# Optimization experiments

Measured on AMD Instinct MI355X. Metric: run time of the kernel, lower is better.

## Reference

```python
import jax, jax.numpy as jnp
import numpy as np

B, N, N_IN, MSG_HID, MSG_OUT, N_HID, N_OUT, K = 32, 128, 16, 64, 64, 64, 16, 4
E = N * (N - 1)  # 16256 directed edges, fully connected w/o self-loops


def setup_inputs() -> dict:
    key = jax.random.key(0)
    ks = jax.random.split(key, 8)
    # one-hot relation matrices (NRI convention)
    rows, cols = np.where(np.ones((N, N)) - np.eye(N))
    eye = np.eye(N, dtype=np.float32)
    rel_rec = jnp.asarray(eye[rows])   # [E, N]
    rel_send = jnp.asarray(eye[cols])  # [E, N]
    s = 0.1  # weight init scale
    return {
        "inputs": jax.random.normal(ks[0], (B, N_IN, N), jnp.float32),
        "rel_rec": rel_rec,
        "rel_send": rel_send,
        "rel_types": jax.nn.softmax(jax.random.normal(ks[1], (B, E, K), jnp.float32), axis=-1),
        "W1": jax.random.normal(ks[2], (K, 2 * N_IN, MSG_HID), jnp.float32) * s,
        "b1": jnp.zeros((K, MSG_HID), jnp.float32),
        "W2": jax.random.normal(ks[3], (K, MSG_HID, MSG_OUT), jnp.float32) * s,
        "b2": jnp.zeros((K, MSG_OUT), jnp.float32),
        "Wo1": jax.random.normal(ks[4], (MSG_OUT + N_IN, N_HID), jnp.float32) * s,
        "bo1": jnp.zeros((N_HID,), jnp.float32),
        "Wo2": jax.random.normal(ks[5], (N_HID, N_HID), jnp.float32) * s,
        "bo2": jnp.zeros((N_HID,), jnp.float32),
        "Wo3": jax.random.normal(ks[6], (N_HID, N_OUT), jnp.float32) * s,
        "bo3": jnp.zeros((N_OUT,), jnp.float32),
    }


def reference(inputs, rel_rec, rel_send, rel_types, W1, b1, W2, b2, Wo1, bo1, Wo2, bo2, Wo3, bo3):
    x = jnp.transpose(inputs, (0, 2, 1))                     # [B, N, n_in]
    senders = jnp.einsum('en,bnf->bef', rel_send, x)          # [B, E, n_in]
    receivers = jnp.einsum('en,bnf->bef', rel_rec, x)         # [B, E, n_in]
    pre_msg = jnp.concatenate([senders, receivers], axis=-1)  # [B, E, 2*n_in]
    all_msgs = jnp.zeros((pre_msg.shape[0], pre_msg.shape[1], W2.shape[-1]), pre_msg.dtype)
    for k in range(W1.shape[0]):  # small fixed loop over edge types
        m = jax.nn.relu(pre_msg @ W1[k] + b1[k])
        m = jax.nn.relu(m @ W2[k] + b2[k])
        all_msgs = all_msgs + m * rel_types[:, :, k:k + 1]
    # edge2node aggregation (no normalization in forward path, matches source)
    agg_msgs = jnp.einsum('bem,en->bnm', all_msgs, rel_rec)   # [B, N, msg_out]
    aug_msgs = jnp.concatenate([x, agg_msgs], axis=-1)        # [B, N, n_in+msg_out]
    h = jax.nn.relu(aug_msgs @ Wo1 + bo1)  # dropout disabled (eval mode)
    h = jax.nn.relu(h @ Wo2 + bo2)
    pred = h @ Wo3 + bo3                                      # [B, N, n_out]
    return jnp.transpose(pred, (0, 2, 1))                     # [B, n_out, N]
```

## Files before the change

### kernel.cpp

```cpp
#include <hip/hip_runtime.h>
#include <stdint.h>

#define B_  32
#define N_  128
#define NIN 16
#define K_  4
#define E_  (N_*(N_-1))

typedef float    f4 __attribute__((ext_vector_type(4)));
typedef _Float16 h8 __attribute__((ext_vector_type(8)));
typedef _Float16 h4 __attribute__((ext_vector_type(4)));

__global__ __launch_bounds__(256) void prep(
    const float* __restrict__ inp, const float* __restrict__ W1,
    const float* __restrict__ b1,  const float* __restrict__ W2,
    const float* __restrict__ Wo1, const float* __restrict__ Wo2,
    const float* __restrict__ Wo3,
    _Float16* __restrict__ Sh, _Float16* __restrict__ Rh,
    _Float16* __restrict__ w2h, _Float16* __restrict__ wn)
{
    const int bid = blockIdx.x;
    const int tid = threadIdx.x;
    if (bid < 1024) {
        int gid = bid*256 + tid;
        int c0 = (gid & 15)*4;
        int n  = (gid >> 4) & 127;
        int b  = (gid >> 11) & 31;
        int k  = gid >> 16;
        f4 s = {0.f,0.f,0.f,0.f};
        f4 r = *(const f4*)(b1 + k*64 + c0);
        const float* xp  = inp + (b*NIN)*N_ + n;
        const f4* w1s = (const f4*)(W1 + (k*32)*64 + c0);
        const f4* w1r = (const f4*)(W1 + (k*32 + 16)*64 + c0);
        #pragma unroll
        for (int f = 0; f < 16; ++f) {
            float xv = xp[f*N_];
            s += xv * w1s[f*16];
            r += xv * w1r[f*16];
        }
        int base = ((k*B_ + b)*N_ + n)*64 + c0;
        h4 sh, rh;
        #pragma unroll
        for (int u = 0; u < 4; ++u) { sh[u] = (_Float16)s[u]; rh[u] = (_Float16)r[u]; }
        *(h4*)(Sh + base) = sh;
        *(h4*)(Rh + base) = rh;
    } else if (bid < 1088) {
        int t = (bid - 1024)*256 + tid;
        int i    = t & 7;
        int lane = (t >> 3) & 63;
        int nt   = (t >> 9) & 3;
        int ks   = (t >> 11) & 1;
        int k    = t >> 12;
        int c = ks*32 + (lane >> 4)*8 + i;
        int o = nt*16 + (lane & 15);
        w2h[t] = (_Float16)W2[(k*64 + c)*64 + o];
    } else {
        int t = (bid - 1088)*256 + tid;
        int j    = t & 7;
        int lane = (t >> 3) & 63;
        int f    = t >> 9;
        int col = lane & 15, q = lane >> 4, row = q*8 + j;
        float v;
        if (f < 12) {
            int ks = f >> 2, nt = f & 3, i = ks*32 + row;
            v = (i < 80) ? Wo1[i*64 + nt*16 + col] : 0.f;
        } else if (f < 20) {
            int g = f - 12, ks = g >> 2, nt = g & 3, i = ks*32 + row;
            v = Wo2[i*64 + nt*16 + col];
        } else {
            int ks = f - 20, i = ks*32 + row;
            v = Wo3[i*16 + col];
        }
        wn[t] = (_Float16)v;
    }
}

__global__ __launch_bounds__(512) void edge_mfma(
    const _Float16* __restrict__ Sh, const _Float16* __restrict__ Rh,
    const _Float16* __restrict__ w2h, const float* __restrict__ rt,
    const float* __restrict__ b2, float* __restrict__ aggK)
{
    __shared__ _Float16 Ssw[N_*64];

    const int tid  = threadIdx.x;
    const int wave = tid >> 6;
    const int lane = tid & 63;
    const int col  = lane & 15;
    const int q    = lane >> 4;
    const int bid  = blockIdx.x;
    const int rt4  = bid & 3;
    const int b    = (bid >> 2) & 31;
    const int k    = bid >> 7;
    const int kb   = k*B_ + b;

    const _Float16* Sg = Sh + (size_t)kb*(N_*64);
    #pragma unroll
    for (int rnd = 0; rnd < 2; ++rnd) {
        int p  = rnd*512 + tid;
        int s  = p >> 3;
        int c8 = (p & 7) ^ (s & 7);
        h8 v = *(const h8*)(Sg + (s*8 + c8)*8);
        *(h8*)(Ssw + p*8) = v;
    }

    const h8* w2v = (const h8*)w2h;
    h8 w2f[2][4];
    #pragma unroll
    for (int ks = 0; ks < 2; ++ks)
        #pragma unroll
        for (int nt = 0; nt < 4; ++nt)
            w2f[ks][nt] = w2v[((k*2 + ks)*4 + nt)*64 + lane];

    f4 b2i[4];
    #pragma unroll
    for (int nt = 0; nt < 4; ++nt) {
        float v = b2[k*64 + nt*16 + col];
        b2i[nt][0] = v; b2i[nt][1] = v; b2i[nt][2] = v; b2i[nt][3] = v;
    }

    __syncthreads();

    const h8* Rv = (const h8*)Rh;
    const h8 zero8 = {0,0,0,0,0,0,0,0};

    #pragma unroll 1
    for (int rg = 0; rg < 4; ++rg) {
        const int r = rt4*32 + wave*4 + rg;
        h8 rf0 = Rv[(kb*N_ + r)*8 + q];
        h8 rf1 = Rv[(kb*N_ + r)*8 + 4 + q];
        const float* rtb = rt + ((size_t)(b*E_ + r*127))*4 + k;

        float aggacc[4] = {0.f, 0.f, 0.f, 0.f};
        #pragma unroll
        for (int mt = 0; mt < 8; ++mt) {
            float rtv[4];
            #pragma unroll
            for (int i = 0; i < 4; ++i) {
                int sdx = mt*16 + q*4 + i;
                float v = 0.f;
                if (sdx != r) v = rtb[(sdx - (sdx > r ? 1 : 0))*4];
                rtv[i] = v;
            }
            int s  = mt*16 + col;
            int x0 = (s*8 + (q       ^ (s & 7)))*8;
            int x1 = (s*8 + ((4 + q) ^ (s & 7)))*8;
            h8 a0 = *(const h8*)(Ssw + x0);
            h8 a1 = *(const h8*)(Ssw + x1);
            a0 = __builtin_elementwise_max(a0 + rf0, zero8);
            a1 = __builtin_elementwise_max(a1 + rf1, zero8);

            #pragma unroll
            for (int nt = 0; nt < 4; ++nt) {
                f4 acc = __builtin_amdgcn_mfma_f32_16x16x32_f16(a0, w2f[0][nt], b2i[nt], 0, 0, 0);
                acc     = __builtin_amdgcn_mfma_f32_16x16x32_f16(a1, w2f[1][nt], acc,    0, 0, 0);
                #pragma unroll
                for (int i = 0; i < 4; ++i)
                    aggacc[nt] += rtv[i] * fmaxf(acc[i], 0.f);
            }
        }
        #pragma unroll
        for (int nt = 0; nt < 4; ++nt) {
            float v = aggacc[nt];
            v += __shfl_xor(v, 16, 64);
            v += __shfl_xor(v, 32, 64);
            if (lane < 16) aggK[((size_t)kb*N_ + r)*64 + nt*16 + lane] = v;
        }
    }
}

__global__ __launch_bounds__(256) void node_mfma(
    const float* __restrict__ aggK, const float* __restrict__ inp,
    const _Float16* __restrict__ wn,
    const float* __restrict__ bo1, const float* __restrict__ bo2,
    const float* __restrict__ bo3, float* __restrict__ out)
{
    __shared__ _Float16 augH[64*128];
    __shared__ _Float16 h12[64*64];

    const int tid = threadIdx.x;
    const int b   = blockIdx.x >> 1;
    const int r0  = (blockIdx.x & 1)*64;

    {
        const int nl = tid >> 2, c4 = tid & 3;
        const int r  = r0 + nl;
        float xv[4];
        #pragma unroll
        for (int u = 0; u < 4; ++u)
            xv[u] = inp[(b*NIN + c4*4 + u)*N_ + r];
        f4 av[4];
        #pragma unroll
        for (int w = 0; w < 4; ++w) {
            int c = w*16 + c4*4;
            f4 a = {0.f,0.f,0.f,0.f};
            #pragma unroll
            for (int k = 0; k < 4; ++k)
                a += *(const f4*)(aggK + (((size_t)k*B_ + b)*N_ + r)*64 + c);
            av[w] = a;
        }
        #pragma unroll
        for (int u = 0; u < 4; ++u) {
            int i = c4*4 + u;
            augH[nl*128 + (((i>>3) ^ (nl&15))<<3) + (i&7)] = (_Float16)xv[u];
        }
        #pragma unroll
        for (int w = 0; w < 4; ++w)
            #pragma unroll
            for (int u = 0; u < 4; ++u) {
                int i = 16 + w*16 + c4*4 + u;
                augH[nl*128 + (((i>>3) ^ (nl&15))<<3) + (i&7)] = (_Float16)av[w][u];
            }
        if (c4 < 2)
            #pragma unroll
            for (int u = 0; u < 8; ++u) {
                int i = 80 + c4*8 + u;
                augH[nl*128 + (((i>>3) ^ (nl&15))<<3) + (i&7)] = (_Float16)0.f;
            }
    }
    __syncthreads();

    const int mt  = tid >> 6, lane = tid & 63;
    const int col = lane & 15, q = lane >> 4;
    const h8* wv   = (const h8*)wn;
    const h8* augV = (const h8*)augH;
    const h8* hv   = (const h8*)h12;
    const int nl   = mt*16 + col;

    f4 acc[4];
    #pragma unroll
    for (int nt = 0; nt < 4; ++nt) {
        float v = bo1[nt*16 + col];
        acc[nt][0] = v; acc[nt][1] = v; acc[nt][2] = v; acc[nt][3] = v;
    }
    #pragma unroll
    for (int ks = 0; ks < 3; ++ks) {
        h8 af = augV[nl*16 + ((ks*4 + q) ^ col)];
        #pragma unroll
        for (int nt = 0; nt < 4; ++nt)
            acc[nt] = __builtin_amdgcn_mfma_f32_16x16x32_f16(af, wv[(ks*4 + nt)*64 + lane], acc[nt], 0, 0, 0);
    }
    #pragma unroll
    for (int nt = 0; nt < 4; ++nt)
        #pragma unroll
        for (int i = 0; i < 4; ++i) {
            int n2 = mt*16 + q*4 + i, o = nt*16 + col;
            h12[n2*64 + (((o>>3) ^ (n2&7))<<3) + (o&7)] = (_Float16)fmaxf(acc[nt][i], 0.f);
        }

    f4 acc2[4];
    #pragma unroll
    for (int nt = 0; nt < 4; ++nt) {
        float v = bo2[nt*16 + col];
        acc2[nt][0] = v; acc2[nt][1] = v; acc2[nt][2] = v; acc2[nt][3] = v;
    }
    #pragma unroll
    for (int ks = 0; ks < 2; ++ks) {
        h8 af = hv[nl*8 + ((ks*4 + q) ^ (col & 7))];
        #pragma unroll
        for (int nt = 0; nt < 4; ++nt)
            acc2[nt] = __builtin_amdgcn_mfma_f32_16x16x32_f16(af, wv[(12 + ks*4 + nt)*64 + lane], acc2[nt], 0, 0, 0);
    }
    #pragma unroll
    for (int nt = 0; nt < 4; ++nt)
        #pragma unroll
        for (int i = 0; i < 4; ++i) {
            int n2 = mt*16 + q*4 + i, o = nt*16 + col;
            h12[n2*64 + (((o>>3) ^ (n2&7))<<3) + (o&7)] = (_Float16)fmaxf(acc2[nt][i], 0.f);
        }

    f4 acc3;
    {
        float v = bo3[col];
        acc3[0] = v; acc3[1] = v; acc3[2] = v; acc3[3] = v;
    }
    #pragma unroll
    for (int ks = 0; ks < 2; ++ks) {
        h8 af = hv[nl*8 + ((ks*4 + q) ^ (col & 7))];
        acc3 = __builtin_amdgcn_mfma_f32_16x16x32_f16(af, wv[(20 + ks)*64 + lane], acc3, 0, 0, 0);
    }
    #pragma unroll
    for (int i = 0; i < 4; ++i) {
        int r = r0 + mt*16 + q*4 + i;
        out[(b*NIN + col)*N_ + r] = acc3[i];
    }
}

extern "C" void kernel_launch(void* const* d_in, const int* in_sizes, int n_in,
                              void* d_out, int out_size, void* d_ws, size_t ws_size,
                              hipStream_t stream)
{
    const float* inp = (const float*)d_in[0];
    const float* rt  = (const float*)d_in[3];
    const float* W1  = (const float*)d_in[4];
    const float* b1  = (const float*)d_in[5];
    const float* W2  = (const float*)d_in[6];
    const float* b2  = (const float*)d_in[7];
    const float* Wo1 = (const float*)d_in[8];
    const float* bo1 = (const float*)d_in[9];
    const float* Wo2 = (const float*)d_in[10];
    const float* bo2 = (const float*)d_in[11];
    const float* Wo3 = (const float*)d_in[12];
    const float* bo3 = (const float*)d_in[13];

    _Float16* Sh   = (_Float16*)d_ws;
    _Float16* Rh   = Sh + (1u << 20);
    _Float16* w2h  = Rh + (1u << 20);
    _Float16* wn   = w2h + 16384;
    float*    aggK = (float*)(wn + 11264);

    hipLaunchKernelGGL(prep, dim3(1132), dim3(256), 0, stream,
                       inp, W1, b1, W2, Wo1, Wo2, Wo3, Sh, Rh, w2h, wn);
    hipLaunchKernelGGL(edge_mfma, dim3(512), dim3(512), 0, stream,
                       Sh, Rh, w2h, rt, b2, aggK);
    hipLaunchKernelGGL(node_mfma, dim3(64), dim3(256), 0, stream,
                       aggK, inp, wn, bo1, bo2, bo3, (float*)d_out);
}
```

Baseline: 143.6 us.

## Pre-transpose rel_types to fp16 per-type dense layout and stage receivers in LDS

The prep kernel gains blocks that convert rel_types from [B,E,K] fp32 (strided by K, with a self-loop gap) into a dense fp16 [K,B,N,N] matrix with explicit zeros on the diagonal. The edge kernel then loads this tile and the receiver rows into shared memory once per block, instead of doing scattered strided global loads with index fixups inside the inner loop. This replaces uncoalesced 4-byte gathers with coalesced vector loads. In exchange it adds a prep pass that writes about 4 MB of fp16 and reads it back, and it rounds the edge weights to fp16.

```diff
diff --git a/kernel.cpp b/kernel.cpp
--- a/kernel.cpp
+++ b/kernel.cpp
@@ -15,9 +15,10 @@
     const float* __restrict__ inp, const float* __restrict__ W1,
     const float* __restrict__ b1,  const float* __restrict__ W2,
     const float* __restrict__ Wo1, const float* __restrict__ Wo2,
-    const float* __restrict__ Wo3,
+    const float* __restrict__ Wo3, const float* __restrict__ rt,
     _Float16* __restrict__ Sh, _Float16* __restrict__ Rh,
-    _Float16* __restrict__ w2h, _Float16* __restrict__ wn)
+    _Float16* __restrict__ w2h, _Float16* __restrict__ wn,
+    _Float16* __restrict__ rtn)
 {
     const int bid = blockIdx.x;
     const int tid = threadIdx.x;
@@ -54,7 +55,7 @@
         int c = ks*32 + (lane >> 4)*8 + i;
         int o = nt*16 + (lane & 15);
         w2h[t] = (_Float16)W2[(k*64 + c)*64 + o];
-    } else {
+    } else if (bid < 1132) {
         int t = (bid - 1088)*256 + tid;
         int j    = t & 7;
         int lane = (t >> 3) & 63;
@@ -72,15 +73,38 @@
             v = Wo3[i*16 + col];
         }
         wn[t] = (_Float16)v;
+    } else {
+        int t = (bid - 1132)*256 + tid;
+        int jg = t & 31;
+        int r  = (t >> 5) & 127;
+        int b  = t >> 12;
+        const f4* rt4p = (const f4*)(rt + (size_t)(b*E_ + r*127)*4);
+        #pragma unroll
+        for (int u = 0; u < 4; ++u) {
+            int j = jg*4 + u;
+            if (j < 127) {
+                f4 v = rt4p[j];
+                int s = j + (j >= r ? 1 : 0);
+                #pragma unroll
+                for (int k = 0; k < 4; ++k)
+                    rtn[((k*B_ + b)*N_ + r)*N_ + s] = (_Float16)v[k];
+            } else {
+                #pragma unroll
+                for (int k = 0; k < 4; ++k)
+                    rtn[((k*B_ + b)*N_ + r)*N_ + r] = (_Float16)0.f;
+            }
+        }
     }
 }
 
 __global__ __launch_bounds__(512) void edge_mfma(
     const _Float16* __restrict__ Sh, const _Float16* __restrict__ Rh,
-    const _Float16* __restrict__ w2h, const float* __restrict__ rt,
+    const _Float16* __restrict__ w2h, const _Float16* __restrict__ rtn,
     const float* __restrict__ b2, float* __restrict__ aggK)
 {
     __shared__ _Float16 Ssw[N_*64];
+    __shared__ _Float16 Rl[32*64];
+    __shared__ _Float16 Rt[32*128];
 
     const int tid  = threadIdx.x;
     const int wave = tid >> 6;
@@ -92,6 +116,7 @@
     const int b    = (bid >> 2) & 31;
     const int k    = bid >> 7;
     const int kb   = k*B_ + b;
+    const int r0   = rt4*32;
 
     const _Float16* Sg = Sh + (size_t)kb*(N_*64);
     #pragma unroll
@@ -99,9 +124,12 @@
         int p  = rnd*512 + tid;
         int s  = p >> 3;
         int c8 = (p & 7) ^ (s & 7);
-        h8 v = *(const h8*)(Sg + (s*8 + c8)*8);
-        *(h8*)(Ssw + p*8) = v;
-    }
+        *(h8*)(Ssw + p*8) = *(const h8*)(Sg + (s*8 + c8)*8);
+    }
+    if (tid < 256)
+        *(h8*)(Rl + tid*8) = *(const h8*)(Rh + ((size_t)kb*N_ + r0)*64 + tid*8);
+    *(h8*)(Rt + tid*8) =
+        *(const h8*)(rtn + ((size_t)kb*N_ + r0)*N_ + tid*8);
 
     const h8* w2v = (const h8*)w2h;
     h8 w2f[2][4];
@@ -120,27 +148,22 @@
 
     __syncthreads();
 
-    const h8* Rv = (const h8*)Rh;
     const h8 zero8 = {0,0,0,0,0,0,0,0};
 
     #pragma unroll 1
     for (int rg = 0; rg < 4; ++rg) {
-        const int r = rt4*32 + wave*4 + rg;
-        h8 rf0 = Rv[(kb*N_ + r)*8 + q];
-        h8 rf1 = Rv[(kb*N_ + r)*8 + 4 + q];
-        const float* rtb = rt + ((size_t)(b*E_ + r*127))*4 + k;
+        const int rl = wave*4 + rg;
+        const int r  = r0 + rl;
+        h8 rf0 = *(const h8*)(Rl + rl*64 + q*8);
+        h8 rf1 = *(const h8*)(Rl + rl*64 + (4 + q)*8);
+        h4 rth[8];
+        #pragma unroll
+        for (int mt = 0; mt < 8; ++mt)
+            rth[mt] = *(const h4*)(Rt + rl*128 + mt*16 + q*4);
 
         float aggacc[4] = {0.f, 0.f, 0.f, 0.f};
         #pragma unroll
         for (int mt = 0; mt < 8; ++mt) {
-            float rtv[4];
-            #pragma unroll
-            for (int i = 0; i < 4; ++i) {
-                int sdx = mt*16 + q*4 + i;
-                float v = 0.f;
-                if (sdx != r) v = rtb[(sdx - (sdx > r ? 1 : 0))*4];
-                rtv[i] = v;
-            }
             int s  = mt*16 + col;
             int x0 = (s*8 + (q       ^ (s & 7)))*8;
             int x1 = (s*8 + ((4 + q) ^ (s & 7)))*8;
@@ -148,6 +171,9 @@
             h8 a1 = *(const h8*)(Ssw + x1);
             a0 = __builtin_elementwise_max(a0 + rf0, zero8);
             a1 = __builtin_elementwise_max(a1 + rf1, zero8);
+            float rtv[4];
+            #pragma unroll
+            for (int i = 0; i < 4; ++i) rtv[i] = (float)rth[mt][i];
 
             #pragma unroll
             for (int nt = 0; nt < 4; ++nt) {
@@ -306,12 +332,13 @@
     _Float16* Rh   = Sh + (1u << 20);
     _Float16* w2h  = Rh + (1u << 20);
     _Float16* wn   = w2h + 16384;
-    float*    aggK = (float*)(wn + 11264);
-
-    hipLaunchKernelGGL(prep, dim3(1132), dim3(256), 0, stream,
-                       inp, W1, b1, W2, Wo1, Wo2, Wo3, Sh, Rh, w2h, wn);
+    _Float16* rtn  = wn + 11264;
+    float*    aggK = (float*)(rtn + (1u << 21));
+
+    hipLaunchKernelGGL(prep, dim3(1644), dim3(256), 0, stream,
+                       inp, W1, b1, W2, Wo1, Wo2, Wo3, rt, Sh, Rh, w2h, wn, rtn);
     hipLaunchKernelGGL(edge_mfma, dim3(512), dim3(512), 0, stream,
-                       Sh, Rh, w2h, rt, b2, aggK);
+                       Sh, Rh, w2h, rtn, b2, aggK);
     hipLaunchKernelGGL(node_mfma, dim3(64), dim3(256), 0, stream,
                        aggK, inp, wn, bo1, bo2, bo3, (float*)d_out);
 }
```

After: 137.7 us. -4.1%, faster.
